# Kernel optimization log

Measured on AMD Instinct MI355X. Metric: run time of the kernel, lower is better.

## Reference

```python
import jax, jax.numpy as jnp
import numpy as np

R_MAX = 10.0
NUM_BESSEL = 8
POLY_P = 5
EMB = 64
MLP_DIM = 256
NUM_LAYERS = 3
IN_DIM = 10
OUT_DIM = 1
N_NODES = 256
N_EDGES = 1024
N_GRAPHS = 16
# gated TP output: 0e channel carries 64 scalars + 128 gates (one per gated 1o/2e irrep)
GATE_MUL = {0: 3 * EMB, 1: EMB, 2: EMB}
L0_PATHS = [(0, 0, 0), (0, 1, 1), (0, 2, 2)]  # in_irreps = 64x0e
LN_PATHS = [(0, 0, 0), (1, 1, 0), (2, 2, 0), (0, 1, 1), (1, 0, 1), (1, 2, 1), (2, 1, 1), (0, 2, 2), (2, 0, 2), (1, 1, 2), (2, 2, 2)]

def _npaths(paths):
    d = {0: 0, 1: 0, 2: 0}
    for _, _, l3 in paths:
        d[l3] += 1
    return d

L0_NP = _npaths(L0_PATHS)
LN_NP = _npaths(LN_PATHS)
L0_NUMEL = sum(EMB * GATE_MUL[l3] for _, _, l3 in L0_PATHS)   # 20480
LN_NUMEL = sum(EMB * GATE_MUL[l3] for _, _, l3 in LN_PATHS)   # 69632

# ---- real spherical harmonics, component normalization (||Y_l||^2 = 2l+1) ----
def _sh_np(v):
    x, y, z = v[:, 0], v[:, 1], v[:, 2]
    s15 = np.sqrt(15.0)
    return {0: np.ones((v.shape[0], 1)),
            1: np.sqrt(3.0) * np.stack([x, y, z], 1),
            2: np.stack([s15 * x * y, s15 * y * z, 0.5 * np.sqrt(5.0) * (3 * z * z - 1), s15 * x * z, 0.5 * s15 * (x * x - y * y)], 1)}

def _rot(axis, t):
    c, s = np.cos(t), np.sin(t)
    R = np.eye(3)
    i, j = [(1, 2), (2, 0), (0, 1)][axis]
    R[i, i] = c; R[j, j] = c; R[i, j] = -s; R[j, i] = s
    return R

_PTS = np.random.RandomState(0).randn(64, 3)
_PTS /= np.linalg.norm(_PTS, axis=1, keepdims=True)

def _D(l, R):
    # rep matrix D with Y(Rv) = D @ Y(v), fit by least squares over sample points
    A = _sh_np(_PTS)[l]
    B = _sh_np(_PTS @ R.T)[l]
    return np.linalg.lstsq(A, B, rcond=None)[0].T

def _gen(l, axis, eps=1e-4):
    return (_D(l, _rot(axis, eps)) - _D(l, _rot(axis, -eps))) / (2 * eps)

def _cg(l1, l2, l3):
    # Clebsch-Gordan tensor as null space of the infinitesimal equivariance constraint
    d1, d2, d3 = 2 * l1 + 1, 2 * l2 + 1, 2 * l3 + 1
    rows = []
    for a in range(3):
        J1, J2, J3 = _gen(l1, a), _gen(l2, a), _gen(l3, a)
        rows.append(np.kron(J1.T, np.eye(d2 * d3)) + np.kron(np.eye(d1), np.kron(J2.T, np.eye(d3))) - np.kron(np.eye(d1 * d2), J3))
    _, _, Vh = np.linalg.svd(np.vstack(rows))
    c = Vh[-1].reshape(d1, d2, d3)
    c = c / np.linalg.norm(c)
    c = c * np.sign(c.flat[int(np.argmax(np.abs(c)))])
    return c

CG = {p: jnp.asarray(_cg(*p), jnp.float32) for p in set(LN_PATHS)}

def _sh_jax(u):
    x, y, z = u[..., 0], u[..., 1], u[..., 2]
    s15 = 15.0 ** 0.5
    return {0: jnp.ones_like(x)[:, None],
            1: (3.0 ** 0.5) * jnp.stack([x, y, z], -1),
            2: jnp.stack([s15 * x * y, s15 * y * z, 0.5 * (5.0 ** 0.5) * (3 * z * z - 1), s15 * x * z, 0.5 * s15 * (x * x - y * y)], -1)}

def _radial(r):
    # Bessel radial basis * polynomial cutoff envelope (MACE-style RadialEmbeddingBlock)
    n = jnp.arange(1, NUM_BESSEL + 1, dtype=r.dtype)
    bessel = (2.0 / R_MAX) ** 0.5 * jnp.sin(n * jnp.pi * r[:, None] / R_MAX) / r[:, None]
    x = r / R_MAX
    p = POLY_P
    env = 1.0 - 0.5 * (p + 1) * (p + 2) * x ** p + p * (p + 2) * x ** (p + 1) - 0.5 * p * (p + 1) * x ** (p + 2)
    env = env * (x < 1.0)
    return bessel * env[:, None]

def _conv(h, sh, ef, recv, send, paths, n_per, w1, b1, w2, b2):
    # TensorProductConvLayer: MLP(edge_feats) -> TP weights, CG tensor product, scatter-sum, gate
    E = ef.shape[0]
    w = jax.nn.relu(ef @ w1 + b1) @ w2 + b2  # (E, weight_numel)
    msgs = {0: 0.0, 1: 0.0, 2: 0.0}
    off = 0
    for (l1, l2, l3) in paths:
        mv = GATE_MUL[l3]
        wp = w[:, off:off + EMB * mv].reshape(E, EMB, mv)
        off += EMB * mv
        tmp = jnp.einsum('eui,ej,ijk->euk', h[l1][send], sh[l2], CG[(l1, l2, l3)])
        alpha = float(1.0 / np.sqrt(EMB * n_per[l3]))  # fan-in path normalization
        msgs[l3] = msgs[l3] + alpha * jnp.einsum('euk,euv->evk', tmp, wp)
    agg = {l: jax.ops.segment_sum(msgs[l], recv, num_segments=N_NODES) for l in msgs}
    s = agg[0][..., 0]  # (N, 192): 64 scalars + 128 gates
    return {0: jax.nn.silu(s[:, :EMB])[:, :, None],
            1: agg[1] * jax.nn.sigmoid(s[:, EMB:2 * EMB])[:, :, None],
            2: agg[2] * jax.nn.sigmoid(s[:, 2 * EMB:])[:, :, None]}

def _forward(atoms, pos, edge_index, batch, emb, l0_fc1_w, l0_fc1_b, l0_fc2_w, l0_fc2_b, fcs1_w, fcs1_b, fcs2_w, fcs2_b, pred_w1, pred_b1, pred_w2, pred_b2):
    recv, send = edge_index[0], edge_index[1]
    vec = pos[recv] - pos[send]
    r = jnp.maximum(jnp.linalg.norm(vec, axis=-1), 1e-6)
    sh = _sh_jax(vec / r[:, None])
    ef = _radial(r)
    h = {0: emb[atoms][:, :, None]}  # (N, 64, 1) scalar features
    h_new = _conv(h, sh, ef, recv, send, L0_PATHS, L0_NP, l0_fc1_w, l0_fc1_b, l0_fc2_w, l0_fc2_b)
    h_new[0] = h_new[0] + h[0]  # residual; F.pad means only scalar block overlaps
    h = h_new
    for i in range(NUM_LAYERS - 1):
        h_new = _conv(h, sh, ef, recv, send, LN_PATHS, LN_NP, fcs1_w[i], fcs1_b[i], fcs2_w[i], fcs2_b[i])
        h = {l: h_new[l] + h[l] for l in h_new}
    pooled = jax.ops.segment_sum(h[0][..., 0], batch, num_segments=N_GRAPHS)  # out[:, :emb_dim]
    return jax.nn.relu(pooled @ pred_w1 + pred_b1) @ pred_w2 + pred_b2

def setup_inputs():
    key = jax.random.key(0)
    ks = jax.random.split(key, 12)
    def lin(k, fi, fo):
        return jax.random.normal(k, (fi, fo), jnp.float32) * float(1.0 / np.sqrt(fi))
    return dict(
        atoms=jax.random.randint(ks[0], (N_NODES,), 0, IN_DIM),
        pos=jax.random.normal(ks[1], (N_NODES, 3), jnp.float32) * 2.0,
        edge_index=jax.random.randint(ks[2], (2, N_EDGES), 0, N_NODES),
        batch=jnp.sort(jax.random.randint(ks[3], (N_NODES,), 0, N_GRAPHS)),
        emb=jax.random.normal(ks[4], (IN_DIM, EMB), jnp.float32),
        l0_fc1_w=lin(ks[5], NUM_BESSEL, MLP_DIM), l0_fc1_b=jnp.zeros((MLP_DIM,), jnp.float32),
        l0_fc2_w=lin(ks[6], MLP_DIM, L0_NUMEL), l0_fc2_b=jnp.zeros((L0_NUMEL,), jnp.float32),
        fcs1_w=jax.random.normal(ks[7], (NUM_LAYERS - 1, NUM_BESSEL, MLP_DIM), jnp.float32) * float(1.0 / np.sqrt(NUM_BESSEL)),
        fcs1_b=jnp.zeros((NUM_LAYERS - 1, MLP_DIM), jnp.float32),
        fcs2_w=jax.random.normal(ks[8], (NUM_LAYERS - 1, MLP_DIM, LN_NUMEL), jnp.float32) * float(1.0 / np.sqrt(MLP_DIM)),
        fcs2_b=jnp.zeros((NUM_LAYERS - 1, LN_NUMEL), jnp.float32),
        pred_w1=lin(ks[9], EMB, EMB), pred_b1=jnp.zeros((EMB,), jnp.float32),
        pred_w2=lin(ks[10], EMB, OUT_DIM), pred_b2=jnp.zeros((OUT_DIM,), jnp.float32),
    )

def reference(atoms, pos, edge_index, batch, emb, l0_fc1_w, l0_fc1_b, l0_fc2_w, l0_fc2_b, fcs1_w, fcs1_b, fcs2_w, fcs2_b, pred_w1, pred_b1, pred_w2, pred_b2):
    return _forward(atoms, pos, edge_index, batch, emb, l0_fc1_w, l0_fc1_b, l0_fc2_w, l0_fc2_b, fcs1_w, fcs1_b, fcs2_w, fcs2_b, pred_w1, pred_b1, pred_w2, pred_b2)
```

## Files before the change

### kernel.cpp

```cpp
#include <hip/hip_runtime.h>
#include <hip/hip_bf16.h>
#include <math.h>

#define NE 1024
#define NN 256
#define NG 16
#define EMB 64
#define KD 256
#define BK 64
#define NUMEL_L0 20480
#define NUMEL_LN 69632
#define MSGW 704
#define MAXE 256

typedef __attribute__((ext_vector_type(8))) __bf16 bf16x8;
typedef __attribute__((ext_vector_type(4))) float f32x4;
typedef __attribute__((ext_vector_type(4))) unsigned int u32x4;

__device__ __align__(16) float g_sh[NE * 8];
__device__ __align__(16) float g_ef[NE * 8];
__device__ __align__(16) unsigned short g_hidb[NE * KD];
__device__ __align__(16) unsigned short g_w2t[(size_t)NUMEL_LN * KD];
__device__ __align__(16) unsigned short g_wb[(size_t)NE * NUMEL_LN];
__device__ __align__(16) float g_msgs[NE * MSGW];
__device__ __align__(16) float g_h0[NN * EMB];
__device__ __align__(16) float g_h1[NN * EMB * 3];
__device__ __align__(16) float g_h2[NN * EMB * 5];
__device__ int g_elist[NN * MAXE];
__device__ int g_ecnt[NN];
__device__ float g_cg[363];

__device__ __forceinline__ unsigned short f2b(float x) {
    __hip_bfloat16 h = __float2bfloat16(x);
    return *(unsigned short*)&h;
}
__device__ __forceinline__ float b2f(unsigned short u) {
    __hip_bfloat16 h;
    *(unsigned short*)&h = u;
    return __bfloat162float(h);
}

__device__ __forceinline__ void gld16(const void* g, void* l) {
    __builtin_amdgcn_global_load_lds(
        (const __attribute__((address_space(1))) unsigned int*)g,
        (__attribute__((address_space(3))) unsigned int*)l, 16, 0, 0);
}

struct Path { int l1, l2, d1, d2, d3, mv, off, cgoff, tmpoff; };

__constant__ Path PLN[11] = {
    {0, 0, 1, 1, 1, 192, 0,     0,   0},
    {1, 1, 3, 3, 1, 192, 12288, 1,   64},
    {2, 2, 5, 5, 1, 192, 24576, 10,  128},
    {0, 1, 1, 3, 3, 64,  36864, 35,  192},
    {1, 0, 3, 1, 3, 64,  40960, 44,  384},
    {1, 2, 3, 5, 3, 64,  45056, 53,  576},
    {2, 1, 5, 3, 3, 64,  49152, 98,  768},
    {0, 2, 1, 5, 5, 64,  53248, 143, 960},
    {2, 0, 5, 1, 5, 64,  57344, 168, 1280},
    {1, 1, 3, 3, 5, 64,  61440, 193, 1600},
    {2, 2, 5, 5, 5, 64,  65536, 238, 1920},
};
__constant__ Path PL0[3] = {
    {0, 0, 1, 1, 1, 192, 0,     0,   0},
    {0, 1, 1, 3, 3, 64,  12288, 35,  64},
    {0, 2, 1, 5, 5, 64,  16384, 143, 256},
};

__device__ void init_cg_body() {
    for (int i = 0; i < 363; i++) g_cg[i] = 0.f;
    const float K3 = 0.57735026918962576f;
    const float K5 = 0.44721359549995794f;
    const float A  = 0.31622776601683794f;
    const float B  = 0.18257418583505536f;
    const float C2 = 0.36514837167011072f;
    const float P  = 0.23904572186687872f;
    const float Q  = 0.20701966780270626f;
    const float S  = 0.11952286093343936f;
    g_cg[0] = 1.f;
    for (int i = 0; i < 3; i++) g_cg[1 + i * 3 + i] = K3;
    for (int i = 0; i < 5; i++) g_cg[10 + i * 5 + i] = K5;
    for (int i = 0; i < 3; i++) g_cg[35 + i * 3 + i] = K3;
    for (int i = 0; i < 3; i++) g_cg[44 + i * 3 + i] = K3;
    g_cg[53 + 1]  = A;  g_cg[53 + 15] = A;  g_cg[53 + 20] = A;
    g_cg[53 + 34] = A;  g_cg[53 + 11] = A;  g_cg[53 + 39] = A;
    g_cg[53 + 6]  = -B; g_cg[53 + 22] = -B; g_cg[53 + 38] = C2;
    g_cg[53 + 12] = A;  g_cg[53 + 28] = -A;
    g_cg[98 + 1]  = A;  g_cg[98 + 3]  = A;  g_cg[98 + 14] = A;
    g_cg[98 + 16] = A;  g_cg[98 + 29] = A;  g_cg[98 + 33] = A;
    g_cg[98 + 18] = -B; g_cg[98 + 22] = -B; g_cg[98 + 26] = C2;
    g_cg[98 + 36] = A;  g_cg[98 + 40] = -A;
    for (int i = 0; i < 5; i++) g_cg[143 + i * 5 + i] = K5;
    for (int i = 0; i < 5; i++) g_cg[168 + i * 5 + i] = K5;
    g_cg[193 + 5]  = A;  g_cg[193 + 15] = A;  g_cg[193 + 26] = A;
    g_cg[193 + 36] = A;  g_cg[193 + 13] = A;  g_cg[193 + 33] = A;
    g_cg[193 + 2]  = -B; g_cg[193 + 22] = -B; g_cg[193 + 42] = C2;
    g_cg[193 + 4]  = A;  g_cg[193 + 24] = -A;
    g_cg[238 + 2]   = P;  g_cg[238 + 10]  = P;  g_cg[238 + 50]  = P;
    g_cg[238 + 8]   = -Q; g_cg[238 + 16]  = -Q; g_cg[238 + 28]  = -Q;
    g_cg[238 + 40]  = -Q; g_cg[238 + 76]  = -Q; g_cg[238 + 80]  = -Q;
    g_cg[238 + 32]  = -S; g_cg[238 + 36]  = -S; g_cg[238 + 56]  = -S;
    g_cg[238 + 34]  = Q;  g_cg[238 + 46]  = Q;  g_cg[238 + 106] = Q;
    g_cg[238 + 62]  = -P;
    g_cg[238 + 74]  = P;  g_cg[238 + 114] = P;  g_cg[238 + 122] = P;
    g_cg[238 + 68]  = -S; g_cg[238 + 88]  = -S; g_cg[238 + 92]  = -S;
    g_cg[238 + 94]  = -Q; g_cg[238 + 98]  = -Q; g_cg[238 + 118] = -Q;
}

__global__ __launch_bounds__(256) void k_setup(const int* ei, const float* pos,
                                               const int* atoms, const float* emb) {
    int bid = blockIdx.x, tid = threadIdx.x;
    if (bid == 0) {
        if (tid == 0) init_cg_body();
        return;
    }
    if (bid <= 4) {
        int e = (bid - 1) * 256 + tid;
        int recv = ei[e], send = ei[NE + e];
        float vx = pos[recv * 3 + 0] - pos[send * 3 + 0];
        float vy = pos[recv * 3 + 1] - pos[send * 3 + 1];
        float vz = pos[recv * 3 + 2] - pos[send * 3 + 2];
        float rn = sqrtf(vx * vx + vy * vy + vz * vz);
        float r = fmaxf(rn, 1e-6f);
        float x = vx / r, y = vy / r, z = vz / r;
        const float S3 = 1.7320508075688772f;
        const float S15 = 3.8729833462074170f;
        const float S5H = 1.1180339887498949f;
        const float S15H = 1.9364916731037085f;
        g_sh[e * 8 + 0] = S3 * x;
        g_sh[e * 8 + 1] = S3 * y;
        g_sh[e * 8 + 2] = S3 * z;
        g_sh[e * 8 + 3] = S15 * x * y;
        g_sh[e * 8 + 4] = S15 * y * z;
        g_sh[e * 8 + 5] = S5H * (3.f * z * z - 1.f);
        g_sh[e * 8 + 6] = S15 * x * z;
        g_sh[e * 8 + 7] = S15H * (x * x - y * y);
        float xr = r * 0.1f;
        float env = 0.f;
        if (xr < 1.f) {
            float x5 = xr * xr * xr * xr * xr;
            env = 1.f - 21.f * x5 + 35.f * x5 * xr - 15.f * x5 * xr * xr;
        }
        const float SB = 0.44721359549995794f;
        const float PI = 3.14159265358979323846f;
        for (int nb = 1; nb <= 8; nb++) {
            g_ef[e * 8 + nb - 1] = SB * sinf((float)nb * PI * r * 0.1f) / r * env;
        }
        return;
    }
    if (bid <= 68) {
        int idx = (bid - 5) * 256 + tid;
        int n = idx / EMB, u = idx % EMB;
        g_h0[idx] = emb[atoms[n] * EMB + u];
        for (int k = 0; k < 3; k++) g_h1[idx * 3 + k] = 0.f;
        for (int k = 0; k < 5; k++) g_h2[idx * 5 + k] = 0.f;
        return;
    }
    {
        int n = bid - 69;
        int lane = tid & 63, w = tid >> 6;
        __shared__ int wsum[4];
        int mask = 0;
#pragma unroll
        for (int i = 0; i < 4; i++) {
            if (ei[tid * 4 + i] == n) mask |= 1 << i;
        }
        int nm = __popc(mask);
        int incl = nm;
#pragma unroll
        for (int off = 1; off < 64; off <<= 1) {
            int v = __shfl_up(incl, off);
            if (lane >= off) incl += v;
        }
        if (lane == 63) wsum[w] = incl;
        __syncthreads();
        int wbase = 0;
        for (int i = 0; i < w; i++) wbase += wsum[i];
        int base = wbase + incl - nm;
#pragma unroll
        for (int i = 0; i < 4; i++) {
            if (mask & (1 << i)) g_elist[n * MAXE + base++] = tid * 4 + i;
        }
        if (tid == 255) g_ecnt[n] = wbase + incl;
    }
}

__global__ __launch_bounds__(256) void k_w2t_hid(const float* w2, int numel,
                                                 const float* w1, const float* b1) {
    __shared__ float t[32][33];
    int bid = blockIdx.x;
    int nw2 = (numel >> 5) << 3;
    if (bid < nw2) {
        int n0 = (bid >> 3) * 32, k0 = (bid & 7) * 32;
        int tx = threadIdx.x & 31, ty = threadIdx.x >> 5;
#pragma unroll
        for (int i = 0; i < 4; i++) {
            int kl = ty * 4 + i;
            t[kl][tx] = w2[(size_t)(k0 + kl) * numel + n0 + tx];
        }
        __syncthreads();
#pragma unroll
        for (int i = 0; i < 4; i++) {
            int nl = ty * 4 + i;
            g_w2t[(size_t)(n0 + nl) * KD + k0 + tx] = f2b(t[tx][nl]);
        }
    } else {
        int e = bid - nw2, m = threadIdx.x;
        float acc = b1[m];
        for (int nb = 0; nb < 8; nb++) acc += g_ef[e * 8 + nb] * w1[nb * KD + m];
        g_hidb[e * KD + m] = f2b(fmaxf(acc, 0.f));
    }
}

__global__ __launch_bounds__(256) void k_gemm_mfma(const float* b2, int numel) {
    __shared__ unsigned short S[16384];
    int tid = threadIdx.x;
    int lane = tid & 63, wid = tid >> 6;
    int wm = wid >> 1, wn = wid & 1;
    int id = blockIdx.x;
    int xcd = id & 7;
    int q = id >> 3;
    int mb = q & 7;
    int ytile = q >> 3;
    int nt = xcd + 8 * ytile;
    int m0 = mb * 128, n0 = nt * 128;
    int fr = lane & 15;
    int ko = (lane >> 4) * 8;

    const char* gA = (const char*)g_hidb;
    const char* gB = (const char*)g_w2t;
    f32x4 acc[4][4] = {};

    for (int kst = 0; kst < 4; kst++) {
#pragma unroll
        for (int i = 0; i < 4; i++) {
            int L = wid * 4096 + i * 1024 + lane * 16;
            int row = L >> 7, p = L & 127;
            int sp = p ^ ((row & 7) << 4);
            gld16(gA + ((size_t)(m0 + row) * KD + kst * BK) * 2 + sp, (char*)S + L);
        }
#pragma unroll
        for (int i = 0; i < 4; i++) {
            int L = wid * 4096 + i * 1024 + lane * 16;
            int row = L >> 7, p = L & 127;
            int sp = p ^ ((row & 7) << 4);
            gld16(gB + ((size_t)(n0 + row) * KD + kst * BK) * 2 + sp, (char*)S + 16384 + L);
        }
        __syncthreads();
#pragma unroll
        for (int ks = 0; ks < 2; ks++) {
            int klb = ks * 64 + ko * 2;
            bf16x8 af[4], bf_[4];
#pragma unroll
            for (int f = 0; f < 4; f++) {
                int ra = wm * 64 + f * 16 + fr;
                af[f] = *(bf16x8*)((char*)S + ra * 128 + (klb ^ ((ra & 7) << 4)));
                int rb = wn * 64 + f * 16 + fr;
                bf_[f] = *(bf16x8*)((char*)S + 16384 + rb * 128 + (klb ^ ((rb & 7) << 4)));
            }
#pragma unroll
            for (int i = 0; i < 4; i++)
#pragma unroll
                for (int j = 0; j < 4; j++)
                    acc[i][j] = __builtin_amdgcn_mfma_f32_16x16x32_bf16(af[i], bf_[j], acc[i][j], 0, 0, 0);
        }
        __syncthreads();
    }

#pragma unroll
    for (int j = 0; j < 4; j++) {
        int colL = wn * 64 + j * 16 + fr;
        float bb = b2[n0 + colL];
#pragma unroll
        for (int i = 0; i < 4; i++) {
#pragma unroll
            for (int r = 0; r < 4; r++) {
                int rowL = wm * 64 + i * 16 + (lane >> 4) * 4 + r;
                *(unsigned short*)((char*)S + rowL * 256 + ((colL * 2) ^ ((rowL & 7) << 4))) =
                    f2b(acc[i][j][r] + bb);
            }
        }
    }
    __syncthreads();
    for (int c = tid; c < 2048; c += 256) {
        int row = c >> 4, p16 = (c & 15) * 16;
        u32x4 v = *(u32x4*)((char*)S + row * 256 + (p16 ^ ((row & 7) << 4)));
        *(u32x4*)((char*)(g_wb + (size_t)(m0 + row) * numel + n0) + p16) = v;
    }
}

__global__ __launch_bounds__(256) void k_contract(const int* ei, int numel, int layer0) {
    int e = blockIdx.x;
    int tid = threadIdx.x;
    __shared__ float sh[8];
    __shared__ float tmp[2240];
    __shared__ __align__(16) unsigned short wlds[64 * 192];
    int send = ei[NE + e];
    if (tid < 8) sh[tid] = g_sh[e * 8 + tid];
    __syncthreads();
    const Path* PT = layer0 ? PL0 : PLN;
    int npaths = layer0 ? 3 : 11;
    int tmptot = layer0 ? 576 : 2240;
    for (int t = tid; t < tmptot; t += 256) {
        int p = npaths - 1;
        while (t < PT[p].tmpoff) p--;
        Path pp = PT[p];
        int rem = t - pp.tmpoff;
        int u = rem / pp.d3, k = rem % pp.d3;
        float acc = 0.f;
        for (int i = 0; i < pp.d1; i++) {
            float hv = (pp.l1 == 0) ? g_h0[send * EMB + u]
                     : (pp.l1 == 1) ? g_h1[(send * EMB + u) * 3 + i]
                                    : g_h2[(send * EMB + u) * 5 + i];
            for (int j = 0; j < pp.d2; j++) {
                float sv = (pp.l2 == 0) ? 1.f : (pp.l2 == 1 ? sh[j] : sh[3 + j]);
                acc += hv * sv * g_cg[pp.cgoff + (i * pp.d2 + j) * pp.d3 + k];
            }
        }
        tmp[t] = acc;
    }
    __syncthreads();
    const unsigned short* wrow = g_wb + (size_t)e * numel;
    float alpha0 = layer0 ? 0.125f : 0.07216878364870323f;
    float alpha12 = layer0 ? 0.125f : 0.0625f;
    int g0 = layer0 ? 1 : 3, g1 = layer0 ? 2 : 7;
    float a0 = 0.f, a1 = 0.f, a2 = 0.f, a3 = 0.f, a4 = 0.f;
    for (int p = 0; p < npaths; p++) {
        Path pp = PT[p];
        if (p == 0 || p == g0 || p == g1) { a0 = a1 = a2 = a3 = a4 = 0.f; }
        {
            int cnt16 = (64 * pp.mv) >> 3;
            const char* src = (const char*)(wrow + pp.off);
            for (int c = tid; c < cnt16; c += 256)
                gld16(src + c * 16, (char*)wlds + c * 16);
        }
        __syncthreads();
        if (tid < pp.mv) {
            int to = pp.tmpoff;
            if (pp.d3 == 1) {
                for (int u = 0; u < 64; u++)
                    a0 += tmp[to + u] * b2f(wlds[u * 192 + tid]);
            } else if (pp.d3 == 3) {
                for (int u = 0; u < 64; u++) {
                    float wv = b2f(wlds[u * 64 + tid]);
                    a0 += tmp[to + u * 3 + 0] * wv;
                    a1 += tmp[to + u * 3 + 1] * wv;
                    a2 += tmp[to + u * 3 + 2] * wv;
                }
            } else {
                for (int u = 0; u < 64; u++) {
                    float wv = b2f(wlds[u * 64 + tid]);
                    a0 += tmp[to + u * 5 + 0] * wv;
                    a1 += tmp[to + u * 5 + 1] * wv;
                    a2 += tmp[to + u * 5 + 2] * wv;
                    a3 += tmp[to + u * 5 + 3] * wv;
                    a4 += tmp[to + u * 5 + 4] * wv;
                }
            }
        }
        __syncthreads();
        if (p == g0 - 1 && tid < 192) {
            g_msgs[e * MSGW + tid] = alpha0 * a0;
        }
        if (p == g1 - 1 && tid < 64) {
            g_msgs[e * MSGW + 192 + tid * 3 + 0] = alpha12 * a0;
            g_msgs[e * MSGW + 192 + tid * 3 + 1] = alpha12 * a1;
            g_msgs[e * MSGW + 192 + tid * 3 + 2] = alpha12 * a2;
        }
        if (p == npaths - 1 && tid < 64) {
            g_msgs[e * MSGW + 384 + tid * 5 + 0] = alpha12 * a0;
            g_msgs[e * MSGW + 384 + tid * 5 + 1] = alpha12 * a1;
            g_msgs[e * MSGW + 384 + tid * 5 + 2] = alpha12 * a2;
            g_msgs[e * MSGW + 384 + tid * 5 + 3] = alpha12 * a3;
            g_msgs[e * MSGW + 384 + tid * 5 + 4] = alpha12 * a4;
        }
    }
}

__global__ __launch_bounds__(256) void k_agggate() {
    int n = blockIdx.x, tid = threadIdx.x;
    __shared__ float agg[MSGW];
    int cnt = g_ecnt[n];
    for (int d = tid; d < MSGW; d += 256) {
        float a = 0.f;
        for (int idx = 0; idx < cnt; idx++) {
            int e = g_elist[n * MAXE + idx];
            a += g_msgs[e * MSGW + d];
        }
        agg[d] = a;
    }
    __syncthreads();
    if (tid < EMB) {
        int u = tid;
        float s0 = agg[u], s1 = agg[64 + u], s2 = agg[128 + u];
        float sg0 = 1.f / (1.f + expf(-s0));
        float g0 = s0 * sg0;
        float sg1 = 1.f / (1.f + expf(-s1));
        float sg2 = 1.f / (1.f + expf(-s2));
        g_h0[n * EMB + u] += g0;
        for (int k = 0; k < 3; k++) g_h1[(n * EMB + u) * 3 + k] += agg[192 + u * 3 + k] * sg1;
        for (int k = 0; k < 5; k++) g_h2[(n * EMB + u) * 5 + k] += agg[384 + u * 5 + k] * sg2;
    }
}

__global__ __launch_bounds__(1024) void k_poolhead(const int* batch, const float* w1,
                                                   const float* b1, const float* w2,
                                                   const float* b2, float* out) {
    __shared__ float pl[NG * EMB];
    int g = threadIdx.x >> 6, u = threadIdx.x & 63;
    float a = 0.f;
    for (int n = 0; n < NN; n++)
        if (batch[n] == g) a += g_h0[n * EMB + u];
    pl[g * EMB + u] = a;
    __syncthreads();
    float t = b1[u];
    for (int uu = 0; uu < EMB; uu++) t += pl[g * EMB + uu] * w1[uu * EMB + u];
    t = fmaxf(t, 0.f);
    float contrib = t * w2[u];
    for (int off = 32; off > 0; off >>= 1) contrib += __shfl_down(contrib, off);
    if (u == 0) out[g] = contrib + b2[0];
}

extern "C" void kernel_launch(void* const* d_in, const int* in_sizes, int n_in,
                              void* d_out, int out_size, void* d_ws, size_t ws_size,
                              hipStream_t stream) {
    const int* atoms = (const int*)d_in[0];
    const float* pos = (const float*)d_in[1];
    const int* ei = (const int*)d_in[2];
    const int* batch = (const int*)d_in[3];
    const float* emb = (const float*)d_in[4];
    const float* l0w1 = (const float*)d_in[5];
    const float* l0b1 = (const float*)d_in[6];
    const float* l0w2 = (const float*)d_in[7];
    const float* l0b2 = (const float*)d_in[8];
    const float* f1w = (const float*)d_in[9];
    const float* f1b = (const float*)d_in[10];
    const float* f2w = (const float*)d_in[11];
    const float* f2b = (const float*)d_in[12];
    const float* pw1 = (const float*)d_in[13];
    const float* pb1 = (const float*)d_in[14];
    const float* pw2 = (const float*)d_in[15];
    const float* pb2 = (const float*)d_in[16];
    float* out = (float*)d_out;

    k_setup<<<dim3(325), dim3(256), 0, stream>>>(ei, pos, atoms, emb);

    for (int layer = 0; layer < 3; layer++) {
        const float* w1 = layer == 0 ? l0w1 : f1w + (size_t)(layer - 1) * 8 * KD;
        const float* b1 = layer == 0 ? l0b1 : f1b + (size_t)(layer - 1) * KD;
        const float* w2 = layer == 0 ? l0w2 : f2w + (size_t)(layer - 1) * KD * NUMEL_LN;
        const float* b2 = layer == 0 ? l0b2 : f2b + (size_t)(layer - 1) * NUMEL_LN;
        int numel = layer == 0 ? NUMEL_L0 : NUMEL_LN;
        int layer0 = layer == 0 ? 1 : 0;
        k_w2t_hid<<<dim3((numel / 32) * 8 + NE), dim3(256), 0, stream>>>(w2, numel, w1, b1);
        k_gemm_mfma<<<dim3((numel / 128) * (NE / 128)), dim3(256), 0, stream>>>(b2, numel);
        k_contract<<<dim3(NE), dim3(256), 0, stream>>>(ei, numel, layer0);
        k_agggate<<<dim3(NN), dim3(256), 0, stream>>>();
    }

    k_poolhead<<<dim3(1), dim3(1024), 0, stream>>>(batch, pw1, pb1, pw2, pb2, out);
}
```

Measured before the change: 430.6 us.

## Double-buffer path weights in contract kernel and spread outputs across all threads

The contract kernel now double-buffers the per-path bf16 weight slab in LDS. It loads the next path's weights while the current path is computed, and issues the first load before the tmp contraction. It also flattens the l=1 and l=2 outputs so each thread computes one output component instead of 64 threads computing 3 or 5 each. This puts 192 to 256 threads to work per path and cuts one barrier per iteration. The cost is doubled weight LDS, which may lower occupancy, and sh values are now read directly from global memory.

```diff
diff --git a/kernel.cpp b/kernel.cpp
--- a/kernel.cpp
+++ b/kernel.cpp
@@ -292,15 +292,22 @@
 __global__ __launch_bounds__(256) void k_contract(const int* ei, int numel, int layer0) {
     int e = blockIdx.x;
     int tid = threadIdx.x;
-    __shared__ float sh[8];
     __shared__ float tmp[2240];
-    __shared__ __align__(16) unsigned short wlds[64 * 192];
-    int send = ei[NE + e];
-    if (tid < 8) sh[tid] = g_sh[e * 8 + tid];
-    __syncthreads();
+    __shared__ __align__(16) unsigned short wlds[2][64 * 192];
     const Path* PT = layer0 ? PL0 : PLN;
     int npaths = layer0 ? 3 : 11;
     int tmptot = layer0 ? 576 : 2240;
+    const unsigned short* wrow = g_wb + (size_t)e * numel;
+
+    {
+        Path pp = PT[0];
+        int cnt16 = (64 * pp.mv) >> 3;
+        const char* src = (const char*)(wrow + pp.off);
+        for (int c = tid; c < cnt16; c += 256)
+            gld16(src + c * 16, (char*)wlds[0] + c * 16);
+    }
+
+    int send = ei[NE + e];
     for (int t = tid; t < tmptot; t += 256) {
         int p = npaths - 1;
         while (t < PT[p].tmpoff) p--;
@@ -313,67 +320,63 @@
                      : (pp.l1 == 1) ? g_h1[(send * EMB + u) * 3 + i]
                                     : g_h2[(send * EMB + u) * 5 + i];
             for (int j = 0; j < pp.d2; j++) {
-                float sv = (pp.l2 == 0) ? 1.f : (pp.l2 == 1 ? sh[j] : sh[3 + j]);
+                float sv = (pp.l2 == 0) ? 1.f
+                         : (pp.l2 == 1 ? g_sh[e * 8 + j] : g_sh[e * 8 + 3 + j]);
                 acc += hv * sv * g_cg[pp.cgoff + (i * pp.d2 + j) * pp.d3 + k];
             }
         }
         tmp[t] = acc;
     }
     __syncthreads();
-    const unsigned short* wrow = g_wb + (size_t)e * numel;
+
     float alpha0 = layer0 ? 0.125f : 0.07216878364870323f;
     float alpha12 = layer0 ? 0.125f : 0.0625f;
     int g0 = layer0 ? 1 : 3, g1 = layer0 ? 2 : 7;
-    float a0 = 0.f, a1 = 0.f, a2 = 0.f, a3 = 0.f, a4 = 0.f;
+    int v3 = tid / 3, k3 = tid - v3 * 3;
+    int v5a = tid / 5, k5a = tid - v5a * 5;
+    int p5b = 256 + tid;
+    int v5b = p5b / 5, k5b = p5b - v5b * 5;
+    float a0 = 0.f, a1 = 0.f;
+    int cur = 0;
+
     for (int p = 0; p < npaths; p++) {
         Path pp = PT[p];
-        if (p == 0 || p == g0 || p == g1) { a0 = a1 = a2 = a3 = a4 = 0.f; }
-        {
-            int cnt16 = (64 * pp.mv) >> 3;
-            const char* src = (const char*)(wrow + pp.off);
+        if (p == 0 || p == g0 || p == g1) { a0 = 0.f; a1 = 0.f; }
+        if (p + 1 < npaths) {
+            Path pn = PT[p + 1];
+            int cnt16 = (64 * pn.mv) >> 3;
+            const char* src = (const char*)(wrow + pn.off);
             for (int c = tid; c < cnt16; c += 256)
-                gld16(src + c * 16, (char*)wlds + c * 16);
+                gld16(src + c * 16, (char*)wlds[cur ^ 1] + c * 16);
+        }
+        const unsigned short* wb = wlds[cur];
+        int to = pp.tmpoff;
+        if (pp.d3 == 1) {
+            if (tid < 192) {
+                for (int u = 0; u < 64; u++)
+                    a0 += tmp[to + u] * b2f(wb[u * 192 + tid]);
+            }
+        } else if (pp.d3 == 3) {
+            if (tid < 192) {
+                for (int u = 0; u < 64; u++)
+                    a0 += tmp[to + u * 3 + k3] * b2f(wb[u * 64 + v3]);
+            }
+        } else {
+            for (int u = 0; u < 64; u++)
+                a0 += tmp[to + u * 5 + k5a] * b2f(wb[u * 64 + v5a]);
+            if (tid < 64) {
+                for (int u = 0; u < 64; u++)
+                    a1 += tmp[to + u * 5 + k5b] * b2f(wb[u * 64 + v5b]);
+            }
+        }
+        if (p == g0 - 1 && tid < 192) g_msgs[e * MSGW + tid] = alpha0 * a0;
+        if (p == g1 - 1 && tid < 192) g_msgs[e * MSGW + 192 + tid] = alpha12 * a0;
+        if (p == npaths - 1) {
+            g_msgs[e * MSGW + 384 + tid] = alpha12 * a0;
+            if (tid < 64) g_msgs[e * MSGW + 640 + tid] = alpha12 * a1;
         }
         __syncthreads();
-        if (tid < pp.mv) {
-            int to = pp.tmpoff;
-            if (pp.d3 == 1) {
-                for (int u = 0; u < 64; u++)
-                    a0 += tmp[to + u] * b2f(wlds[u * 192 + tid]);
-            } else if (pp.d3 == 3) {
-                for (int u = 0; u < 64; u++) {
-                    float wv = b2f(wlds[u * 64 + tid]);
-                    a0 += tmp[to + u * 3 + 0] * wv;
-                    a1 += tmp[to + u * 3 + 1] * wv;
-                    a2 += tmp[to + u * 3 + 2] * wv;
-                }
-            } else {
-                for (int u = 0; u < 64; u++) {
-                    float wv = b2f(wlds[u * 64 + tid]);
-                    a0 += tmp[to + u * 5 + 0] * wv;
-                    a1 += tmp[to + u * 5 + 1] * wv;
-                    a2 += tmp[to + u * 5 + 2] * wv;
-                    a3 += tmp[to + u * 5 + 3] * wv;
-                    a4 += tmp[to + u * 5 + 4] * wv;
-                }
-            }
-        }
-        __syncthreads();
-        if (p == g0 - 1 && tid < 192) {
-            g_msgs[e * MSGW + tid] = alpha0 * a0;
-        }
-        if (p == g1 - 1 && tid < 64) {
-            g_msgs[e * MSGW + 192 + tid * 3 + 0] = alpha12 * a0;
-            g_msgs[e * MSGW + 192 + tid * 3 + 1] = alpha12 * a1;
-            g_msgs[e * MSGW + 192 + tid * 3 + 2] = alpha12 * a2;
-        }
-        if (p == npaths - 1 && tid < 64) {
-            g_msgs[e * MSGW + 384 + tid * 5 + 0] = alpha12 * a0;
-            g_msgs[e * MSGW + 384 + tid * 5 + 1] = alpha12 * a1;
-            g_msgs[e * MSGW + 384 + tid * 5 + 2] = alpha12 * a2;
-            g_msgs[e * MSGW + 384 + tid * 5 + 3] = alpha12 * a3;
-            g_msgs[e * MSGW + 384 + tid * 5 + 4] = alpha12 * a4;
-        }
+        cur ^= 1;
     }
 }
 
```

Result: slower. 535.2 us (+24.3%).
